# Optimization experiments

Hardware: AMD Instinct MI355X
Metric: run time of the kernel (lower is better)

## Reference

```python
import jax, jax.numpy as jnp
import numpy as np

NIN = 512
HID = 512
T = 512
B = 64
INITRANGE = 0.1


def setup_inputs() -> dict:
    key = jax.random.key(0)
    ks = jax.random.split(key, 6)
    x = jax.random.normal(ks[0], (T, B, NIN), dtype=jnp.float32)
    mask = jnp.ones((T, B), dtype=jnp.float32)
    # torch Linear(nin+hidden, hidden): weight [HID, NIN+HID], uniform(-0.1, 0.1), bias zeros
    def lin(k):
        return jax.random.uniform(k, (HID, NIN + HID), dtype=jnp.float32,
                                  minval=-INITRANGE, maxval=INITRANGE)
    return {
        "x": x, "mask": mask,
        "Wf": lin(ks[1]), "bf": jnp.zeros((HID,), jnp.float32),
        "Wi": lin(ks[2]), "bi": jnp.zeros((HID,), jnp.float32),
        "Wc": lin(ks[3]), "bc": jnp.zeros((HID,), jnp.float32),
        "Wo": lin(ks[4]), "bo": jnp.zeros((HID,), jnp.float32),
    }


def reference(x, mask, Wf, bf, Wi, bi, Wc, bc, Wo, bo):
    # Fuse the 4 gate linears into one GEMM per step (same math).
    # Gate order: f, i, o, ctilde
    W = jnp.concatenate([Wf, Wi, Wo, Wc], axis=0)        # [4H, NIN+H]
    b = jnp.concatenate([bf, bi, bo, bc], axis=0)        # [4H]
    H = Wf.shape[0]
    Bsz = x.shape[1]
    h0 = jnp.zeros((Bsz, H), x.dtype)
    c0 = jnp.zeros((Bsz, H), x.dtype)

    def step(carry, inp):
        h, c = carry
        xt, mt = inp                                    # [B, NIN], [B]
        comb = jnp.concatenate([h, xt], axis=1)         # hidden first, as in torch code
        z = comb @ W.T + b                              # [B, 4H]
        f = jax.nn.sigmoid(z[:, 0 * H:1 * H])
        i = jax.nn.sigmoid(z[:, 1 * H:2 * H])
        o = jax.nn.sigmoid(z[:, 2 * H:3 * H])
        c_tilde = jnp.tanh(z[:, 3 * H:4 * H])
        m = mt[:, None]
        c_new = f * c + i * c_tilde
        c_new = m * c_new + (1.0 - m) * c
        h_new = o * jnp.tanh(c_new)
        h_new = m * h_new + (1.0 - m) * h
        return (h_new, c_new), (h_new, i)

    (_, _), (h_hist, i_hist) = jax.lax.scan(step, (h0, c0), (x, mask))
    return h_hist, i_hist  # each [T, B, H]
```

## Files before the change

kernel.cpp:

```cpp
#include <hip/hip_runtime.h>
#include <math.h>

#define T_STEPS 512
#define BATCH   64
#define HID     512
#define NROW    2048
#define HHIST   16777216ULL

typedef __attribute__((ext_vector_type(8))) short short8_t;
typedef __attribute__((ext_vector_type(4))) float float4_t;
typedef __attribute__((ext_vector_type(4))) unsigned uint4_t;

__device__ __forceinline__ float sigf(float z) {
  z = fminf(fmaxf(z, -30.f), 30.f);
  return 1.f / (1.f + __expf(-z));
}
__device__ __forceinline__ float tanhf_(float v) {
  v = fminf(fmaxf(v, -15.f), 15.f);
  const float e = __expf(2.f * v);
  return (e - 1.f) / (e + 1.f);
}
__device__ __forceinline__ unsigned short bf16hi(float f) {
  unsigned u = __float_as_uint(f);
  return (unsigned short)((u + 0x7fffu + ((u >> 16) & 1u)) >> 16);
}
__device__ __forceinline__ float bf16f(unsigned short h) {
  return __uint_as_float(((unsigned)h) << 16);
}
__device__ __forceinline__ unsigned packh(float f) {
  unsigned short h = bf16hi(f);
  unsigned short l = bf16hi(f - bf16f(h));
  return (((unsigned)h) << 16) | (unsigned)l;
}

__device__ __forceinline__ bool poll_fast(const unsigned long long* hq, unsigned t,
                                          uint4_t& a, uint4_t& b,
                                          uint4_t& c, uint4_t& d) {
  asm volatile(
      "global_load_dwordx4 %0, %4, off sc0\n\t"
      "global_load_dwordx4 %1, %4, off offset:16 sc0\n\t"
      "global_load_dwordx4 %2, %4, off offset:32 sc0\n\t"
      "global_load_dwordx4 %3, %4, off offset:48 sc0\n\t"
      "s_waitcnt vmcnt(0)"
      : "=&v"(a), "=&v"(b), "=&v"(c), "=&v"(d)
      : "v"(hq)
      : "memory");
  return a[1] == t && a[3] == t && b[1] == t && b[3] == t &&
         c[1] == t && c[3] == t && d[1] == t && d[3] == t;
}

__global__ __launch_bounds__(256) void xgemm_kernel(
    const float* __restrict__ x,
    const float* __restrict__ Wf, const float* __restrict__ Wi,
    const float* __restrict__ Wo, const float* __restrict__ Wc,
    const float* __restrict__ bf, const float* __restrict__ bi,
    const float* __restrict__ bo, const float* __restrict__ bc,
    float* __restrict__ Zx)
{
  const int rtile = blockIdx.x;
  const int t     = blockIdx.y;
  const int g  = rtile >> 2;
  const int n0 = (rtile & 3) * 128;
  const float* Wg = (g == 0) ? Wf : (g == 1) ? Wi : (g == 2) ? Wo : Wc;
  const float* bg = (g == 0) ? bf : (g == 1) ? bi : (g == 2) ? bo : bc;

  __shared__ float Wt[32][132];
  __shared__ float Xt[32][68];

  const int tid = threadIdx.x;
  const int tr  = tid & 31;
  const int tb  = tid >> 5;

  float acc[4][8];
#pragma unroll
  for (int i = 0; i < 4; ++i)
#pragma unroll
    for (int j = 0; j < 8; ++j) acc[i][j] = 0.f;

  float biasv[4];
#pragma unroll
  for (int i = 0; i < 4; ++i) biasv[i] = bg[n0 + tr * 4 + i];

  const float* xt = x + (size_t)t * (BATCH * 512);

  for (int kc = 0; kc < 512; kc += 32) {
#pragma unroll
    for (int p = 0; p < 4; ++p) {
      const int r  = p * 32 + (tid >> 3);
      const int kk = (tid & 7) * 4;
      float4 v = *(const float4*)&Wg[(size_t)(n0 + r) * 1024 + 512 + kc + kk];
      Wt[kk + 0][r] = v.x; Wt[kk + 1][r] = v.y;
      Wt[kk + 2][r] = v.z; Wt[kk + 3][r] = v.w;
    }
    {
      const int b  = tid >> 2;
      const int kk = (tid & 3) * 8;
      float4 v0 = *(const float4*)&xt[b * 512 + kc + kk];
      float4 v1 = *(const float4*)&xt[b * 512 + kc + kk + 4];
      Xt[kk + 0][b] = v0.x; Xt[kk + 1][b] = v0.y;
      Xt[kk + 2][b] = v0.z; Xt[kk + 3][b] = v0.w;
      Xt[kk + 4][b] = v1.x; Xt[kk + 5][b] = v1.y;
      Xt[kk + 6][b] = v1.z; Xt[kk + 7][b] = v1.w;
    }
    __syncthreads();
#pragma unroll
    for (int kk = 0; kk < 32; ++kk) {
      float4 wv = *(const float4*)&Wt[kk][tr * 4];
      float4 x0 = *(const float4*)&Xt[kk][tb * 8];
      float4 x1 = *(const float4*)&Xt[kk][tb * 8 + 4];
      const float wa[4] = {wv.x, wv.y, wv.z, wv.w};
      const float xa[8] = {x0.x, x0.y, x0.z, x0.w, x1.x, x1.y, x1.z, x1.w};
#pragma unroll
      for (int i = 0; i < 4; ++i)
#pragma unroll
        for (int j = 0; j < 8; ++j)
          acc[i][j] = fmaf(wa[i], xa[j], acc[i][j]);
    }
    __syncthreads();
  }

  const int rg = g * 512 + n0 + tr * 4;
#pragma unroll
  for (int ir = 0; ir < 4; ++ir) {
    const float bv = biasv[ir];
    float4 o0 = make_float4(acc[ir][0] + bv, acc[ir][1] + bv,
                            acc[ir][2] + bv, acc[ir][3] + bv);
    float4 o1 = make_float4(acc[ir][4] + bv, acc[ir][5] + bv,
                            acc[ir][6] + bv, acc[ir][7] + bv);
    float* dst = Zx + (((size_t)t * 8 + tb) * NROW + rg + ir) * 8;
    *(float4*)dst       = o0;
    *(float4*)(dst + 4) = o1;
  }
}

__global__ __launch_bounds__(512, 2) void lstm_rec_fast(
    const float* __restrict__ mask,
    const float* __restrict__ Wf, const float* __restrict__ Wi,
    const float* __restrict__ Wo, const float* __restrict__ Wc,
    const float* __restrict__ Zx,
    unsigned long long* __restrict__ hP,
    unsigned* __restrict__ xb,
    float* __restrict__ out)
{
  __shared__ __align__(16) short hip_[2][8 * 512];
  __shared__ __align__(16) short lop_[2][8 * 512];
  __shared__ unsigned s_role;

  const int tid  = threadIdx.x;

  if (tid == 0) {
    unsigned xcd;
    asm volatile("s_getreg_b32 %0, hwreg(20, 0, 32)" : "=s"(xcd));
    xcd &= 7u;
    const unsigned slot = __hip_atomic_fetch_add(&xb[xcd], 1u, __ATOMIC_RELAXED,
                                                 __HIP_MEMORY_SCOPE_AGENT);
    __builtin_amdgcn_fence(__ATOMIC_RELEASE, "agent");
    __hip_atomic_fetch_add(&xb[15], 1u, __ATOMIC_RELAXED,
                           __HIP_MEMORY_SCOPE_AGENT);
    const unsigned nwg = gridDim.x;
    while (__hip_atomic_load(&xb[15], __ATOMIC_RELAXED,
                             __HIP_MEMORY_SCOPE_AGENT) < nwg)
      __builtin_amdgcn_s_sleep(2);
    __builtin_amdgcn_fence(__ATOMIC_ACQUIRE, "agent");
    unsigned pfx = 0;
    for (unsigned xx = 0; xx < xcd; ++xx)
      pfx += __hip_atomic_load(&xb[xx], __ATOMIC_RELAXED,
                               __HIP_MEMORY_SCOPE_AGENT);
    s_role = pfx + slot;
  }
  __syncthreads();
  const unsigned role = s_role;
  const int g  = (int)(role >> 4);
  const int n0 = (int)(role & 15u) * 32;

  const int wv   = tid >> 6;
  const int lane = tid & 63;
  const int kq   = lane >> 4;
  const int l15  = lane & 15;

  const int gateA = l15 & 3;
  const int unitA = n0 + wv * 4 + (l15 >> 2);
  const float* WmA =
      (gateA == 0) ? Wf : (gateA == 1) ? Wi : (gateA == 2) ? Wo : Wc;
  const float* WrowA = WmA + (size_t)unitA * 1024;
  short8_t Ahi[16], Alo[16];
#pragma unroll
  for (int it = 0; it < 16; ++it) {
    const int base = it * 32 + kq * 8;
#pragma unroll
    for (int j = 0; j < 8; ++j) {
      const float f = WrowA[base + j];
      const unsigned short h = bf16hi(f);
      Ahi[it][j] = (short)h;
      Alo[it][j] = (short)bf16hi(f - bf16f(h));
    }
  }

  const int unitD = n0 + wv * 4 + kq;
  const int bD    = l15;
  const bool act  = (l15 < 8);
  float c_r = 0.f, h_r = 0.f;

  const int b_s = tid >> 6;
  const int kr  = (tid & 63) * 8;
  const int bcol = l15 & 7;

  bool fastok = true;

  float zxc[4] = {0.f, 0.f, 0.f, 0.f};
  float mvc = 0.f;
  if (act) {
    mvc = mask[g * 8 + bD];
#pragma unroll
    for (int r = 0; r < 4; ++r)
      zxc[r] = Zx[(((size_t)0 * 8 + g) * NROW + r * 512 + unitD) * 8 + bD];
  }

  for (int t = 0; t < T_STEPS; ++t) {
    {
      const unsigned long long* hq =
          hP + (((size_t)(t & 1) * 8 + g) * 8 + b_s) * 512 + kr;
      unsigned p8[8];
      bool got = false;
      if (fastok) {
        uint4_t a, b, c, d;
        for (int it2 = 0; it2 < 64 && !got; ++it2)
          got = poll_fast(hq, (unsigned)t, a, b, c, d);
        if (got) {
          p8[0] = a[0]; p8[1] = a[2]; p8[2] = b[0]; p8[3] = b[2];
          p8[4] = c[0]; p8[5] = c[2]; p8[6] = d[0]; p8[7] = d[2];
        } else {
          fastok = false;
        }
      }
      if (!got) {
        unsigned long long q[8];
        while (true) {
#pragma unroll
          for (int j = 0; j < 8; ++j)
            q[j] = __hip_atomic_load(hq + j, __ATOMIC_RELAXED,
                                     __HIP_MEMORY_SCOPE_AGENT);
          bool ok = true;
#pragma unroll
          for (int j = 0; j < 8; ++j)
            ok &= ((unsigned)(q[j] >> 32) == (unsigned)t);
          if (ok) break;
          __builtin_amdgcn_s_sleep(1);
        }
#pragma unroll
        for (int j = 0; j < 8; ++j) p8[j] = (unsigned)q[j];
      }
      short8_t H, L;
#pragma unroll
      for (int j = 0; j < 8; ++j) {
        H[j] = (short)(p8[j] >> 16);
        L[j] = (short)(p8[j] & 0xffffu);
      }
      const int sOff = b_s * 1024 + ((kr * 2) ^ ((b_s & 7) << 4));
      *(short8_t*)((char*)hip_[t & 1] + sOff) = H;
      *(short8_t*)((char*)lop_[t & 1] + sOff) = L;
    }

    float zxn[4] = {0.f, 0.f, 0.f, 0.f};
    float mvn = 0.f;
    if (act && t + 1 < T_STEPS) {
      mvn = mask[(t + 1) * 64 + g * 8 + bD];
#pragma unroll
      for (int r = 0; r < 4; ++r)
        zxn[r] = Zx[(((size_t)(t + 1) * 8 + g) * NROW + r * 512 + unitD) * 8 + bD];
    }

    __syncthreads();

    float4_t c0 = {0.f, 0.f, 0.f, 0.f};
    float4_t c1 = {0.f, 0.f, 0.f, 0.f};
    float4_t c2 = {0.f, 0.f, 0.f, 0.f};
    {
      const char* hib = (const char*)hip_[t & 1] + bcol * 1024;
      const char* lob = (const char*)lop_[t & 1] + bcol * 1024;
      const int xr = bcol << 4;
#pragma unroll
      for (int it = 0; it < 16; ++it) {
        const int o = it * 64 + kq * 16;
        const short8_t bh = *(const short8_t*)(hib + (o ^ xr));
        const short8_t bl = *(const short8_t*)(lob + (o ^ xr));
        c0 = __builtin_amdgcn_mfma_f32_16x16x32_bf16(Ahi[it], bh, c0, 0, 0, 0);
        c1 = __builtin_amdgcn_mfma_f32_16x16x32_bf16(Ahi[it], bl, c1, 0, 0, 0);
        c2 = __builtin_amdgcn_mfma_f32_16x16x32_bf16(Alo[it], bh, c2, 0, 0, 0);
      }
    }

    if (act) {
      float z[4];
#pragma unroll
      for (int r = 0; r < 4; ++r) z[r] = c0[r] + c1[r] + c2[r] + zxc[r];
      const float f  = sigf(z[0]);
      const float ig = sigf(z[1]);
      const float o  = sigf(z[2]);
      const float ct = tanhf_(z[3]);
      float cn = f * c_r + ig * ct;
      cn = mvc * cn + (1.f - mvc) * c_r;
      c_r = cn;
      float hn = o * tanhf_(cn);
      hn = mvc * hn + (1.f - mvc) * h_r;
      h_r = hn;
      const size_t hidx =
          (((size_t)((t + 1) & 1) * 8 + g) * 8 + bD) * 512 + unitD;
      const unsigned long long pk =
          (((unsigned long long)(unsigned)(t + 1)) << 32) |
          (unsigned long long)packh(hn);
      *(volatile unsigned long long*)(hP + hidx) = pk;
      __hip_atomic_store(hP + hidx, pk, __ATOMIC_RELAXED,
                         __HIP_MEMORY_SCOPE_AGENT);
      const size_t ob = ((size_t)t * 64 + g * 8 + bD) * 512 + unitD;
      out[ob] = hn;
      out[HHIST + ob] = ig;
    }

#pragma unroll
    for (int r = 0; r < 4; ++r) zxc[r] = zxn[r];
    mvc = mvn;
  }
}

__device__ __forceinline__ void grid_barrier(unsigned* cnt, int w, int tid, int round) {
  __syncthreads();
  if (tid == 0) {
    __builtin_amdgcn_fence(__ATOMIC_RELEASE, "agent");
    unsigned* gc = cnt + 16 + ((w >> 4) << 5);
    unsigned prev = __hip_atomic_fetch_add(gc, 1u, __ATOMIC_RELAXED,
                                           __HIP_MEMORY_SCOPE_AGENT);
    if ((prev & 15u) == 15u)
      __hip_atomic_fetch_add(cnt, 1u, __ATOMIC_RELAXED,
                             __HIP_MEMORY_SCOPE_AGENT);
    const unsigned target = (unsigned)(round + 1) * 16u;
    while (__hip_atomic_load(cnt, __ATOMIC_RELAXED,
                             __HIP_MEMORY_SCOPE_AGENT) < target)
      __builtin_amdgcn_s_sleep(2);
    __builtin_amdgcn_fence(__ATOMIC_ACQUIRE, "agent");
  }
  __syncthreads();
}

__global__ __launch_bounds__(512) void lstm_rec_inline(
    const float* __restrict__ x,  const float* __restrict__ mask,
    const float* __restrict__ Wf, const float* __restrict__ Wi,
    const float* __restrict__ Wo, const float* __restrict__ Wc,
    const float* __restrict__ bf, const float* __restrict__ bi,
    const float* __restrict__ bo, const float* __restrict__ bc,
    float* __restrict__ hT, unsigned* __restrict__ cnt,
    float* __restrict__ out)
{
  constexpr int WC = 1024;
  __shared__ float Wlds[8 * WC];
  __shared__ float zpart[8 * 8 * 64];

  const int tid = threadIdx.x;
  const int w   = blockIdx.x;
  const int kq  = tid >> 6;
  const int b   = tid & 63;
  const int n0  = ((w & 7) << 6) + ((w >> 3) << 1);

#pragma unroll
  for (int i = 0; i < WC / 256; ++i) {
    const int idx4 = tid + (i << 9);
    const int rr   = idx4 / (WC / 4);
    const int col  = (idx4 % (WC / 4)) * 4;
    const int g = rr >> 1, u = rr & 1;
    const float* Wrow =
        ((g == 0) ? Wf : (g == 1) ? Wi : (g == 2) ? Wo : Wc) +
        (size_t)(n0 + u) * 1024;
    *(float4*)&Wlds[rr * WC + col] = *(const float4*)&Wrow[col];
  }

  float biasv[4] = {0.f, 0.f, 0.f, 0.f};
  float c_r = 0.f, h_r = 0.f;
  if (tid < 128) {
    const int u = tid >> 6;
    biasv[0] = bf[n0 + u]; biasv[1] = bi[n0 + u];
    biasv[2] = bo[n0 + u]; biasv[3] = bc[n0 + u];
  }
  __syncthreads();

  for (int t = 0; t < T_STEPS; ++t) {
    float zpre[4] = {0.f, 0.f, 0.f, 0.f};
    float mval = 0.f;
    if (tid < 128) {
      const int bb = tid & 63;
      mval = mask[t * 64 + bb];
#pragma unroll
      for (int g = 0; g < 4; ++g) zpre[g] = biasv[g];
    }

    float acc[8];
#pragma unroll
    for (int rr = 0; rr < 8; ++rr) acc[rr] = 0.f;

    {
      const float* hcur = hT + ((t & 1) << 15);
      const int k0 = kq << 6;
#pragma unroll
      for (int k4 = 0; k4 < 16; ++k4) {
        const int k = k0 + (k4 << 2);
        const float h0 = hcur[(k + 0) * 64 + b];
        const float h1 = hcur[(k + 1) * 64 + b];
        const float h2 = hcur[(k + 2) * 64 + b];
        const float h3 = hcur[(k + 3) * 64 + b];
#pragma unroll
        for (int rr = 0; rr < 8; ++rr) {
          float4 wv = *(const float4*)&Wlds[rr * WC + k];
          acc[rr] = fmaf(h0, wv.x, acc[rr]);
          acc[rr] = fmaf(h1, wv.y, acc[rr]);
          acc[rr] = fmaf(h2, wv.z, acc[rr]);
          acc[rr] = fmaf(h3, wv.w, acc[rr]);
        }
      }
    }
    {
      const float* xt = x + (size_t)t * (64 * 512) + b * 512;
      const int k0 = kq << 6;
#pragma unroll
      for (int k4 = 0; k4 < 16; ++k4) {
        const int k = k0 + (k4 << 2);
        float4 xv = *(const float4*)&xt[k];
#pragma unroll
        for (int rr = 0; rr < 8; ++rr) {
          float4 wv = *(const float4*)&Wlds[rr * WC + 512 + k];
          acc[rr] = fmaf(xv.x, wv.x, acc[rr]);
          acc[rr] = fmaf(xv.y, wv.y, acc[rr]);
          acc[rr] = fmaf(xv.z, wv.z, acc[rr]);
          acc[rr] = fmaf(xv.w, wv.w, acc[rr]);
        }
      }
    }

#pragma unroll
    for (int rr = 0; rr < 8; ++rr)
      zpart[((kq << 3) + rr) * 64 + b] = acc[rr];
    __syncthreads();

    if (tid < 128) {
      const int u = tid >> 6, bb = tid & 63;
      float z[4];
#pragma unroll
      for (int g = 0; g < 4; ++g) {
        const int rr = g * 2 + u;
        float s = zpre[g];
#pragma unroll
        for (int q = 0; q < 8; ++q) s += zpart[((q << 3) + rr) * 64 + bb];
        z[g] = s;
      }
      const float f  = sigf(z[0]);
      const float ig = sigf(z[1]);
      const float o  = sigf(z[2]);
      const float ct = tanhf_(z[3]);
      float cn = f * c_r + ig * ct;
      cn = mval * cn + (1.f - mval) * c_r;
      c_r = cn;
      float hn = o * tanhf_(cn);
      hn = mval * hn + (1.f - mval) * h_r;
      h_r = hn;
      const int n = n0 + u;
      hT[(((t + 1) & 1) << 15) + n * 64 + bb] = hn;
      out[((size_t)t * 64 + bb) * 512 + n]         = hn;
      out[HHIST + ((size_t)t * 64 + bb) * 512 + n] = ig;
    }

    if (t != T_STEPS - 1) grid_barrier(cnt, w, tid, t);
  }
}

extern "C" void kernel_launch(void* const* d_in, const int* in_sizes, int n_in,
                              void* d_out, int out_size, void* d_ws, size_t ws_size,
                              hipStream_t stream) {
  (void)in_sizes; (void)n_in; (void)out_size;
  const float* x    = (const float*)d_in[0];
  const float* mask = (const float*)d_in[1];
  const float* Wf   = (const float*)d_in[2];
  const float* bf   = (const float*)d_in[3];
  const float* Wi   = (const float*)d_in[4];
  const float* bi   = (const float*)d_in[5];
  const float* Wc   = (const float*)d_in[6];
  const float* bc   = (const float*)d_in[7];
  const float* Wo   = (const float*)d_in[8];
  const float* bo   = (const float*)d_in[9];
  float* out = (float*)d_out;

  const size_t zx_bytes = (size_t)T_STEPS * NROW * 64 * 4;
  const size_t hp_bytes = (size_t)2 * 8 * 8 * 512 * 8;
  const bool fast = ws_size >= zx_bytes + hp_bytes + 4096;

  if (fast) {
    float* Zx = (float*)d_ws;
    unsigned long long* hP = (unsigned long long*)((char*)d_ws + zx_bytes);
    unsigned* xb = (unsigned*)((char*)hP + hp_bytes);
    hipMemsetAsync(hP, 0, hp_bytes + 4096, stream);
    hipLaunchKernelGGL(xgemm_kernel, dim3(16, 512), dim3(256), 0, stream,
                       x, Wf, Wi, Wo, Wc, bf, bi, bo, bc, Zx);
    void* kargs[] = { (void*)&mask, (void*)&Wf, (void*)&Wi, (void*)&Wo,
                      (void*)&Wc, (void*)&Zx, (void*)&hP, (void*)&xb,
                      (void*)&out };
    hipLaunchCooperativeKernel(reinterpret_cast<void*>(&lstm_rec_fast),
                               dim3(128), dim3(512), kargs, 0, stream);
  } else {
    float* hT = (float*)d_ws;
    const size_t h_bytes = 2 * 64 * 512 * 4;
    unsigned* cnt = (unsigned*)((char*)hT + h_bytes);
    hipMemsetAsync(hT, 0, h_bytes + 4096, stream);
    void* kargs[] = { (void*)&x, (void*)&mask, (void*)&Wf, (void*)&Wi,
                      (void*)&Wo, (void*)&Wc, (void*)&bf, (void*)&bi,
                      (void*)&bo, (void*)&bc, (void*)&hT, (void*)&cnt,
                      (void*)&out };
    hipLaunchCooperativeKernel(reinterpret_cast<void*>(&lstm_rec_inline),
                               dim3(256), dim3(512), kargs, 0, stream);
  }
}
```

Measured before the change: 3.560 ms.

## Add per-wave sentinel flags to gate polling before loading hidden state

```diff
diff --git a/kernel.cpp b/kernel.cpp
--- a/kernel.cpp
+++ b/kernel.cpp
@@ -49,6 +49,15 @@
          c[1] == t && c[3] == t && d[1] == t && d[3] == t;
 }
 
+__device__ __forceinline__ bool sent_fast(const unsigned long long* sq, unsigned t) {
+  uint4_t s4;
+  asm volatile(
+      "global_load_dwordx4 %0, %1, off sc0\n\t"
+      "s_waitcnt vmcnt(0)"
+      : "=&v"(s4) : "v"(sq) : "memory");
+  return s4[1] == t && s4[3] == t;
+}
+
 __global__ __launch_bounds__(256) void xgemm_kernel(
     const float* __restrict__ x,
     const float* __restrict__ Wf, const float* __restrict__ Wi,
@@ -140,6 +149,7 @@
     const float* __restrict__ Zx,
     unsigned long long* __restrict__ hP,
     unsigned* __restrict__ xb,
+    unsigned long long* __restrict__ hS,
     float* __restrict__ out)
 {
   __shared__ __align__(16) short hip_[2][8 * 512];
@@ -171,7 +181,8 @@
   __syncthreads();
   const unsigned role = s_role;
   const int g  = (int)(role >> 4);
-  const int n0 = (int)(role & 15u) * 32;
+  const int m  = (int)(role & 15u);
+  const int n0 = m * 32;
 
   const int wv   = tid >> 6;
   const int lane = tid & 63;
@@ -217,6 +228,29 @@
   }
 
   for (int t = 0; t < T_STEPS; ++t) {
+    {
+      const unsigned long long* sq =
+          hS + (((size_t)(t & 1) * 8 + g) << 7) + 2 * (tid & 63);
+      bool sgot = false;
+      if (fastok) {
+        for (int it2 = 0; it2 < 96 && !sgot; ++it2)
+          sgot = sent_fast(sq, (unsigned)t);
+        if (!sgot) fastok = false;
+      }
+      if (!sgot) {
+        while (true) {
+          unsigned long long s0 = __hip_atomic_load(sq, __ATOMIC_RELAXED,
+                                                    __HIP_MEMORY_SCOPE_AGENT);
+          unsigned long long s1 = __hip_atomic_load(sq + 1, __ATOMIC_RELAXED,
+                                                    __HIP_MEMORY_SCOPE_AGENT);
+          if ((unsigned)(s0 >> 32) == (unsigned)t &&
+              (unsigned)(s1 >> 32) == (unsigned)t)
+            break;
+          __builtin_amdgcn_s_sleep(1);
+        }
+      }
+    }
+
     {
       const unsigned long long* hq =
           hP + (((size_t)(t & 1) * 8 + g) * 8 + b_s) * 512 + kr;
@@ -224,7 +258,7 @@
       bool got = false;
       if (fastok) {
         uint4_t a, b, c, d;
-        for (int it2 = 0; it2 < 64 && !got; ++it2)
+        for (int it2 = 0; it2 < 32 && !got; ++it2)
           got = poll_fast(hq, (unsigned)t, a, b, c, d);
         if (got) {
           p8[0] = a[0]; p8[1] = a[2]; p8[2] = b[0]; p8[3] = b[2];
@@ -312,6 +346,15 @@
       *(volatile unsigned long long*)(hP + hidx) = pk;
       __hip_atomic_store(hP + hidx, pk, __ATOMIC_RELAXED,
                          __HIP_MEMORY_SCOPE_AGENT);
+      if (lane == 0) {
+        unsigned long long* sp =
+            hS + (((size_t)((t + 1) & 1) * 8 + g) << 7) + (m * 8 + wv);
+        const unsigned long long sv =
+            ((unsigned long long)(unsigned)(t + 1)) << 32;
+        *(volatile unsigned long long*)sp = sv;
+        __hip_atomic_store(sp, sv, __ATOMIC_RELAXED,
+                           __HIP_MEMORY_SCOPE_AGENT);
+      }
       const size_t ob = ((size_t)t * 64 + g * 8 + bD) * 512 + unitD;
       out[ob] = hn;
       out[HHIST + ob] = ig;
@@ -488,18 +531,21 @@
 
   const size_t zx_bytes = (size_t)T_STEPS * NROW * 64 * 4;
   const size_t hp_bytes = (size_t)2 * 8 * 8 * 512 * 8;
-  const bool fast = ws_size >= zx_bytes + hp_bytes + 4096;
+  const size_t xb_bytes = 4096;
+  const size_t hs_bytes = (size_t)2 * 8 * 128 * 8;
+  const bool fast = ws_size >= zx_bytes + hp_bytes + xb_bytes + hs_bytes;
 
   if (fast) {
     float* Zx = (float*)d_ws;
     unsigned long long* hP = (unsigned long long*)((char*)d_ws + zx_bytes);
     unsigned* xb = (unsigned*)((char*)hP + hp_bytes);
-    hipMemsetAsync(hP, 0, hp_bytes + 4096, stream);
+    unsigned long long* hS = (unsigned long long*)((char*)xb + xb_bytes);
+    hipMemsetAsync(hP, 0, hp_bytes + xb_bytes + hs_bytes, stream);
     hipLaunchKernelGGL(xgemm_kernel, dim3(16, 512), dim3(256), 0, stream,
                        x, Wf, Wi, Wo, Wc, bf, bi, bo, bc, Zx);
     void* kargs[] = { (void*)&mask, (void*)&Wf, (void*)&Wi, (void*)&Wo,
                       (void*)&Wc, (void*)&Zx, (void*)&hP, (void*)&xb,
-                      (void*)&out };
+                      (void*)&hS, (void*)&out };
     hipLaunchCooperativeKernel(reinterpret_cast<void*>(&lstm_rec_fast),
                                dim3(128), dim3(512), kargs, 0, stream);
   } else {
```

Result: slower. 3.999 ms (+12.3%).
